# Optimization experiments

Hardware: AMD Instinct MI355X
Metric: run time of the kernel (lower is better)

The kernel has to match this reference:

```python
import jax, jax.numpy as jnp
import numpy as np

D = 1024  # in_features
H = 16    # head_num

def setup_inputs() -> dict:
    key = jax.random.key(0)
    ks = jax.random.split(key, 11)
    S, B = 2048, 2
    scale = 1.0 / np.sqrt(D)
    inp = {
        'q': jax.random.normal(ks[0], (S, B, D), jnp.float32),
        'k': jax.random.normal(ks[1], (S, B, D), jnp.float32),
        'v': jax.random.normal(ks[2], (S, B, D), jnp.float32),
        'Wq': jax.random.normal(ks[3], (D, D), jnp.float32) * scale,
        'Wk': jax.random.normal(ks[4], (D, D), jnp.float32) * scale,
        'Wv': jax.random.normal(ks[5], (D, D), jnp.float32) * scale,
        'Wo': jax.random.normal(ks[6], (D, D), jnp.float32) * scale,
        'bq': jax.random.normal(ks[7], (D,), jnp.float32) * 0.01,
        'bk': jax.random.normal(ks[8], (D,), jnp.float32) * 0.01,
        'bv': jax.random.normal(ks[9], (D,), jnp.float32) * 0.01,
        'bo': jax.random.normal(ks[10], (D,), jnp.float32) * 0.01,
    }
    return inp

def reference(q, k, v, Wq, Wk, Wv, Wo, bq, bk, bv, bo):
    # q,k,v: (S, B, D) -> (B, S, D)
    q = jnp.transpose(q, (1, 0, 2))
    k = jnp.transpose(k, (1, 0, 2))
    v = jnp.transpose(v, (1, 0, 2))
    # linear + ReLU (torch Linear: x @ W.T + b)
    qh = jax.nn.relu(q @ Wq.T + bq)
    kh = jax.nn.relu(k @ Wk.T + bk)
    vh = jax.nn.relu(v @ Wv.T + bv)
    B, S, _ = qh.shape
    hd = D // H
    # (B, S, H, hd) -> (B, H, S, hd)
    qh = qh.reshape(B, S, H, hd).transpose(0, 2, 1, 3)
    kh = kh.reshape(B, S, H, hd).transpose(0, 2, 1, 3)
    vh = vh.reshape(B, S, H, hd).transpose(0, 2, 1, 3)
    scores = jnp.einsum('bhsd,bhtd->bhst', qh, kh) / np.sqrt(hd).astype(np.float32)
    attn = jax.nn.softmax(scores, axis=-1)
    y = jnp.einsum('bhst,bhtd->bhsd', attn, vh)  # (B, H, S, hd)
    y = y.transpose(0, 2, 1, 3).reshape(B, S, D)
    y = jax.nn.relu(y @ Wo.T + bo)
    return jnp.transpose(y, (1, 0, 2))  # (S, B, D)
```

## Files before the change

### kernel.cpp

```cpp
#include <hip/hip_runtime.h>
#include <stdint.h>

typedef __attribute__((ext_vector_type(8))) short bf8v;
typedef __attribute__((ext_vector_type(4))) float f4v;
typedef __attribute__((ext_vector_type(16))) float f16v;
typedef __attribute__((ext_vector_type(4))) unsigned int u4v;

__device__ __forceinline__ unsigned short f2bf(float f) {
  unsigned int u = __float_as_uint(f);
  u += 0x7fffu + ((u >> 16) & 1u);
  return (unsigned short)(u >> 16);
}

__device__ __forceinline__ void gload16(const void* g, void* l) {
  __builtin_amdgcn_global_load_lds(
      (__attribute__((address_space(1))) void*)reinterpret_cast<uintptr_t>(g),
      (__attribute__((address_space(3))) void*)reinterpret_cast<uintptr_t>(l),
      16, 0, 0);
}

__device__ __forceinline__ unsigned cvtpk(float lo, float hi) {
  unsigned r;
  asm("v_cvt_pk_bf16_f32 %0, %1, %2" : "=v"(r) : "v"(lo), "v"(hi));
  return r;
}

__global__ __launch_bounds__(256) void cvt_all(
    const float* __restrict__ s0, const float* __restrict__ s1,
    const float* __restrict__ s2, const float* __restrict__ s3,
    const float* __restrict__ s4, const float* __restrict__ s5,
    const float* __restrict__ s6, unsigned short* __restrict__ dst) {
  const size_t NA = (size_t)1 << 22, NW = (size_t)1 << 20;
  size_t i = ((size_t)blockIdx.x * 256 + threadIdx.x) * 8;
  const float* src;
  size_t off;
  if (i < 3 * NA) {
    int a = (int)(i >> 22);
    src = (a == 0) ? s0 : (a == 1) ? s1 : s2;
    off = i & (NA - 1);
  } else {
    size_t j = i - 3 * NA;
    int a = (int)(j >> 20);
    src = (a == 0) ? s3 : (a == 1) ? s4 : (a == 2) ? s5 : s6;
    off = j & (NW - 1);
  }
  const f4v* sp = (const f4v*)(src + off);
  f4v x = sp[0], y = sp[1];
  bf8v r;
  r[0] = (short)f2bf(x[0]); r[1] = (short)f2bf(x[1]);
  r[2] = (short)f2bf(x[2]); r[3] = (short)f2bf(x[3]);
  r[4] = (short)f2bf(y[0]); r[5] = (short)f2bf(y[1]);
  r[6] = (short)f2bf(y[2]); r[7] = (short)f2bf(y[3]);
  *(bf8v*)(dst + i) = r;
}

template <int OMODE>
__device__ __forceinline__ void gemm_body(
    unsigned short* Al, unsigned short* Bl,
    const unsigned short* __restrict__ A, const unsigned short* __restrict__ W,
    const float* __restrict__ bias, void* __restrict__ out) {
  const int tid = threadIdx.x;
  const int w = tid >> 6, l = tid & 63;
  const int lr = l >> 4, lc = l & 15;
  const int m0 = blockIdx.x * 128, n0 = blockIdx.y * 128;
  const int wr = w >> 1, wc = w & 1;

  f4v acc[4][4];
#pragma unroll
  for (int i = 0; i < 4; i++)
#pragma unroll
    for (int j = 0; j < 4; j++) acc[i][j] = (f4v)(0.0f);

  const int NK = 32;
#pragma unroll
  for (int i = 0; i < 2; i++) {
    int chunk = w * 2 + i;
    int e = (chunk * 1024 + l * 16) >> 1;
    int r = e >> 5, k = e & 31;
    gload16(A + (size_t)(m0 + r) * 1024 + k, Al + chunk * 512);
    gload16(W + (size_t)(n0 + r) * 1024 + k, Bl + chunk * 512);
  }

  for (int kk = 0; kk < NK; kk++) {
    const int cur = kk & 1;
    __syncthreads();
    if (kk + 1 < NK) {
#pragma unroll
      for (int i = 0; i < 2; i++) {
        int chunk = w * 2 + i;
        int e = (chunk * 1024 + l * 16) >> 1;
        int r = e >> 5, k = (kk + 1) * 32 + (e & 31);
        gload16(A + (size_t)(m0 + r) * 1024 + k, Al + (cur ^ 1) * 4096 + chunk * 512);
        gload16(W + (size_t)(n0 + r) * 1024 + k, Bl + (cur ^ 1) * 4096 + chunk * 512);
      }
    }
    bf8v av[4], bv[4];
#pragma unroll
    for (int i = 0; i < 4; i++) {
      int row = wr * 64 + i * 16 + lc;
      av[i] = *(const bf8v*)(Al + cur * 4096 + row * 32 + lr * 8);
    }
#pragma unroll
    for (int j = 0; j < 4; j++) {
      int row = wc * 64 + j * 16 + lc;
      bv[j] = *(const bf8v*)(Bl + cur * 4096 + row * 32 + lr * 8);
    }
#pragma unroll
    for (int i = 0; i < 4; i++)
#pragma unroll
      for (int j = 0; j < 4; j++)
        acc[i][j] = __builtin_amdgcn_mfma_f32_16x16x32_bf16(av[i], bv[j], acc[i][j], 0, 0, 0);
  }

#pragma unroll
  for (int j = 0; j < 4; j++) {
    int n = n0 + wc * 64 + j * 16 + lc;
    float bj = bias[n];
#pragma unroll
    for (int i = 0; i < 4; i++) {
      int mb = m0 + wr * 64 + i * 16 + lr * 4;
#pragma unroll
      for (int q = 0; q < 4; q++) {
        float val = fmaxf(acc[i][j][q] + bj, 0.0f);
        int m = mb + q;
        if (OMODE == 2) {
          int s = m & 2047, b = m >> 11;
          ((float*)out)[(size_t)(s * 2 + b) * 1024 + n] = val;
        } else {
          int s = m >> 1, b = m & 1;
          int h = n >> 6, d = n & 63;
          if (OMODE == 0)
            ((unsigned short*)out)[((size_t)(b * 16 + h) * 2048 + s) * 64 + d] = f2bf(val);
          else
            ((unsigned short*)out)[((size_t)(b * 16 + h) * 64 + d) * 2048 + s] = f2bf(val);
        }
      }
    }
  }
}

__global__ __launch_bounds__(256) void qkv_gemm(
    const unsigned short* __restrict__ qA, const unsigned short* __restrict__ kA,
    const unsigned short* __restrict__ vA,
    const unsigned short* __restrict__ Wq, const unsigned short* __restrict__ Wk,
    const unsigned short* __restrict__ Wv,
    const float* __restrict__ bq, const float* __restrict__ bk,
    const float* __restrict__ bv,
    unsigned short* __restrict__ Qh, unsigned short* __restrict__ Kh,
    unsigned short* __restrict__ Vt) {
  __shared__ __align__(16) unsigned short Al[2 * 4096];
  __shared__ __align__(16) unsigned short Bl[2 * 4096];
  int z = blockIdx.z;
  if (z == 0)      gemm_body<0>(Al, Bl, qA, Wq, bq, Qh);
  else if (z == 1) gemm_body<0>(Al, Bl, kA, Wk, bk, Kh);
  else             gemm_body<1>(Al, Bl, vA, Wv, bv, Vt);
}

__global__ __launch_bounds__(256) void out_gemm(
    const unsigned short* __restrict__ Y, const unsigned short* __restrict__ Wo,
    const float* __restrict__ bo, float* __restrict__ out) {
  __shared__ __align__(16) unsigned short Al[2 * 4096];
  __shared__ __align__(16) unsigned short Bl[2 * 4096];
  gemm_body<2>(Al, Bl, Y, Wo, bo, out);
}

__global__ __launch_bounds__(256, 2) void attn_kernel(
    const unsigned short* __restrict__ Qh, const unsigned short* __restrict__ Kh,
    const unsigned short* __restrict__ Vt, unsigned short* __restrict__ Y) {
  __shared__ __align__(16) unsigned short Kl[2][4096];
  __shared__ __align__(16) unsigned short Vl[2][4096];
  const int tid = threadIdx.x, w = tid >> 6, l = tid & 63;
  const int lo = l & 31, hi = l >> 5;
  const int bh = blockIdx.y;
  const int q0 = blockIdx.x * 128 + w * 32;
  const size_t qkbase = (size_t)bh * 2048 * 64;
  const size_t vtbase = (size_t)bh * 64 * 2048;
  const float cs = 0.125f * 1.44269504088896341f;

  bf8v qf[4];
#pragma unroll
  for (int c = 0; c < 4; c++)
    qf[c] = *(const bf8v*)(Qh + qkbase + (size_t)(q0 + lo) * 64 + c * 16 + hi * 8);

  f16v oacc[2];
  oacc[0] = (f16v)(0.0f);
  oacc[1] = (f16v)(0.0f);
  float mrun = -1e30f, lrun = 0.0f;

  const int swl = (lo & 7) << 4;
  int akb[4], avb[2][2][2];
#pragma unroll
  for (int c = 0; c < 4; c++) akb[c] = lo * 128 + ((c * 32 + hi * 16) ^ swl);
#pragma unroll
  for (int dt = 0; dt < 2; dt++)
#pragma unroll
    for (int kvh = 0; kvh < 2; kvh++)
#pragma unroll
      for (int kc = 0; kc < 2; kc++)
        avb[dt][kvh][kc] = (dt * 32 + lo) * 128 + ((kvh * 64 + kc * 32 + hi * 16) ^ swl);

  int stE[2], stD[2], stKV[2];
#pragma unroll
  for (int i = 0; i < 2; i++) {
    int o = (w * 2 + i) * 1024 + l * 16;
    int row = o >> 7;
    stE[i] = (o ^ ((row & 7) << 4)) >> 1;
    stD[i] = stE[i] >> 6;
    stKV[i] = stE[i] & 63;
  }
  const char* KlB = (const char*)&Kl[0][0];
  const char* VlB = (const char*)&Vl[0][0];

  auto STAGE = [&](int buf, int t0) {
#pragma unroll
    for (int i = 0; i < 2; i++) {
      gload16(Kh + qkbase + (size_t)t0 * 64 + stE[i], (char*)&Kl[buf][0] + (w * 2 + i) * 1024);
      gload16(Vt + vtbase + (size_t)stD[i] * 2048 + t0 + stKV[i], (char*)&Vl[buf][0] + (w * 2 + i) * 1024);
    }
  };

  auto COMPUTE = [&](int bo) {
#pragma unroll
    for (int kvh = 0; kvh < 2; kvh++) {
      bf8v kf[4];
#pragma unroll
      for (int c = 0; c < 4; c++)
        kf[c] = *(const bf8v*)(KlB + bo + kvh * 4096 + akb[c]);
      f16v sc16 = (f16v)(0.0f);
#pragma unroll
      for (int c = 0; c < 4; c++)
        sc16 = __builtin_amdgcn_mfma_f32_32x32x16_bf16(kf[c], qf[c], sc16, 0, 0, 0);
      bf8v vf[2][2];
#pragma unroll
      for (int dt = 0; dt < 2; dt++)
#pragma unroll
        for (int kc = 0; kc < 2; kc++)
          vf[dt][kc] = *(const bf8v*)(VlB + bo + avb[dt][kvh][kc]);

      float m0a = fmaxf(fmaxf(sc16[0], sc16[1]), sc16[2]);
      float m0b = fmaxf(fmaxf(sc16[3], sc16[4]), sc16[5]);
      float m0c = fmaxf(fmaxf(sc16[6], sc16[7]), sc16[8]);
      float m0d = fmaxf(fmaxf(sc16[9], sc16[10]), sc16[11]);
      float m0e = fmaxf(fmaxf(sc16[12], sc16[13]), sc16[14]);
      float m16 = fmaxf(fmaxf(fmaxf(m0a, m0b), fmaxf(m0c, m0d)), fmaxf(m0e, sc16[15]));
      m16 = fmaxf(m16, __shfl_xor(m16, 32));
      float msc = m16 * cs;
      if (!__all(msc <= mrun + 8.0f)) {
        float mnew = fmaxf(mrun, msc);
        float scl = __builtin_amdgcn_exp2f(mrun - mnew);
        lrun *= scl;
#pragma unroll
        for (int dt = 0; dt < 2; dt++)
#pragma unroll
          for (int r = 0; r < 16; r++) oacc[dt][r] *= scl;
        mrun = mnew;
      }
      float p[16];
      float rs = 0.0f;
#pragma unroll
      for (int r = 0; r < 16; r++) {
        p[r] = __builtin_amdgcn_exp2f(sc16[r] * cs - mrun);
        rs += p[r];
      }
      rs += __shfl_xor(rs, 32);
      lrun += rs;
      bf8v pf[2];
#pragma unroll
      for (int kc = 0; kc < 2; kc++) {
        unsigned a0 = cvtpk(p[kc * 8 + 0], p[kc * 8 + 1]);
        unsigned a1 = cvtpk(p[kc * 8 + 2], p[kc * 8 + 3]);
        unsigned b0 = cvtpk(p[kc * 8 + 4], p[kc * 8 + 5]);
        unsigned b1 = cvtpk(p[kc * 8 + 6], p[kc * 8 + 7]);
        asm("v_permlane32_swap_b32 %0, %1" : "+v"(a0), "+v"(b0));
        asm("v_permlane32_swap_b32 %0, %1" : "+v"(a1), "+v"(b1));
        u4v pw;
        pw[0] = a0; pw[1] = a1; pw[2] = b0; pw[3] = b1;
        pf[kc] = __builtin_bit_cast(bf8v, pw);
      }
#pragma unroll
      for (int dt = 0; dt < 2; dt++)
#pragma unroll
        for (int kc = 0; kc < 2; kc++)
          oacc[dt] = __builtin_amdgcn_mfma_f32_32x32x16_bf16(vf[dt][kc], pf[kc], oacc[dt], 0, 0, 0);
    }
  };

  STAGE(0, 0);
  __syncthreads();
#pragma unroll 1
  for (int t0 = 0; t0 < 2048; t0 += 128) {
    STAGE(1, t0 + 64);
    COMPUTE(0);
    __syncthreads();
    if (t0 + 128 < 2048) STAGE(0, t0 + 128);
    COMPUTE(8192);
    __syncthreads();
  }

  const int b = bh >> 4, h = bh & 15;
  {
    float inv = 1.0f / lrun;
    int q = q0 + lo;
    size_t base = ((size_t)(b * 2048 + q) << 10) + h * 64;
#pragma unroll
    for (int dt = 0; dt < 2; dt++)
#pragma unroll
      for (int r = 0; r < 16; r++) {
        int d = dt * 32 + (r & 3) + 8 * (r >> 2) + 4 * hi;
        Y[base + d] = f2bf(oacc[dt][r] * inv);
      }
  }
}

extern "C" void kernel_launch(void* const* d_in, const int* in_sizes, int n_in,
                              void* d_out, int out_size, void* d_ws, size_t ws_size,
                              hipStream_t stream) {
  const float* q  = (const float*)d_in[0];
  const float* k  = (const float*)d_in[1];
  const float* v  = (const float*)d_in[2];
  const float* Wq = (const float*)d_in[3];
  const float* Wk = (const float*)d_in[4];
  const float* Wv = (const float*)d_in[5];
  const float* Wo = (const float*)d_in[6];
  const float* bq = (const float*)d_in[7];
  const float* bk = (const float*)d_in[8];
  const float* bv = (const float*)d_in[9];
  const float* bo = (const float*)d_in[10];

  const size_t NA = (size_t)4096 * 1024;
  const size_t NW = (size_t)1024 * 1024;
  unsigned short* qA  = (unsigned short*)d_ws;
  unsigned short* kA  = qA  + NA;
  unsigned short* vA  = kA  + NA;
  unsigned short* WqB = vA  + NA;
  unsigned short* WkB = WqB + NW;
  unsigned short* WvB = WkB + NW;
  unsigned short* WoB = WvB + NW;
  unsigned short* Qh  = WoB + NW;
  unsigned short* Kh  = Qh  + NA;
  unsigned short* Vt  = Kh  + NA;
  unsigned short* Y   = Vt  + NA;

  cvt_all<<<dim3(8192), 256, 0, stream>>>(q, k, v, Wq, Wk, Wv, Wo, qA);

  qkv_gemm<<<dim3(32, 8, 3), 256, 0, stream>>>(qA, kA, vA, WqB, WkB, WvB,
                                               bq, bk, bv, Qh, Kh, Vt);
  attn_kernel<<<dim3(16, 32), 256, 0, stream>>>(Qh, Kh, Vt, Y);
  out_gemm<<<dim3(32, 8), 256, 0, stream>>>(Y, WoB, bo, (float*)d_out);
}
```

Baseline: 128.5 us.

## Split attention over key range with combine kernel; narrow out_gemm tile

Attention is split into two halves along the key dimension (grid z=2), doubling the block count from 512 to 1024. Each half writes unnormalized partial outputs plus running max/sum, and a new combine kernel merges them into Y. The output GEMM now uses a 64-wide N tile to double its grid, and attention launch bounds request 4 blocks per SM. The aim is better CU occupancy on a 256-CU part, at the cost of an extra kernel launch, extra partial-result traffic, and bf16 rounding of the unnormalized partials.

Measured after the change: 132.3 us. 2.9% more time.

```diff
diff --git a/kernel.cpp b/kernel.cpp
--- a/kernel.cpp
+++ b/kernel.cpp
@@ -10,6 +10,10 @@
   unsigned int u = __float_as_uint(f);
   u += 0x7fffu + ((u >> 16) & 1u);
   return (unsigned short)(u >> 16);
+}
+
+__device__ __forceinline__ float bf2f(unsigned short s) {
+  return __uint_as_float((unsigned)s << 16);
 }
 
 __device__ __forceinline__ void gload16(const void* g, void* l) {
@@ -54,7 +58,7 @@
   *(bf8v*)(dst + i) = r;
 }
 
-template <int OMODE>
+template <int OMODE, int TN>
 __device__ __forceinline__ void gemm_body(
     unsigned short* Al, unsigned short* Bl,
     const unsigned short* __restrict__ A, const unsigned short* __restrict__ W,
@@ -62,22 +66,31 @@
   const int tid = threadIdx.x;
   const int w = tid >> 6, l = tid & 63;
   const int lr = l >> 4, lc = l & 15;
-  const int m0 = blockIdx.x * 128, n0 = blockIdx.y * 128;
+  const int m0 = blockIdx.x * 128, n0 = blockIdx.y * TN;
   const int wr = w >> 1, wc = w & 1;
-
-  f4v acc[4][4];
+  const int JW = TN / 32;
+  const int BCPW = TN / 64;
+  const int BBUF = TN * 32;
+
+  f4v acc[4][JW];
 #pragma unroll
   for (int i = 0; i < 4; i++)
 #pragma unroll
-    for (int j = 0; j < 4; j++) acc[i][j] = (f4v)(0.0f);
+    for (int j = 0; j < JW; j++) acc[i][j] = (f4v)(0.0f);
 
   const int NK = 32;
 #pragma unroll
   for (int i = 0; i < 2; i++) {
     int chunk = w * 2 + i;
-    int e = (chunk * 1024 + l * 16) >> 1;
+    int e = chunk * 512 + l * 8;
     int r = e >> 5, k = e & 31;
     gload16(A + (size_t)(m0 + r) * 1024 + k, Al + chunk * 512);
+  }
+#pragma unroll
+  for (int i = 0; i < BCPW; i++) {
+    int chunk = w * BCPW + i;
+    int e = chunk * 512 + l * 8;
+    int r = e >> 5, k = e & 31;
     gload16(W + (size_t)(n0 + r) * 1024 + k, Bl + chunk * 512);
   }
 
@@ -88,33 +101,39 @@
 #pragma unroll
       for (int i = 0; i < 2; i++) {
         int chunk = w * 2 + i;
-        int e = (chunk * 1024 + l * 16) >> 1;
+        int e = chunk * 512 + l * 8;
         int r = e >> 5, k = (kk + 1) * 32 + (e & 31);
         gload16(A + (size_t)(m0 + r) * 1024 + k, Al + (cur ^ 1) * 4096 + chunk * 512);
-        gload16(W + (size_t)(n0 + r) * 1024 + k, Bl + (cur ^ 1) * 4096 + chunk * 512);
-      }
-    }
-    bf8v av[4], bv[4];
+      }
+#pragma unroll
+      for (int i = 0; i < BCPW; i++) {
+        int chunk = w * BCPW + i;
+        int e = chunk * 512 + l * 8;
+        int r = e >> 5, k = (kk + 1) * 32 + (e & 31);
+        gload16(W + (size_t)(n0 + r) * 1024 + k, Bl + (cur ^ 1) * BBUF + chunk * 512);
+      }
+    }
+    bf8v av[4], bv[JW];
 #pragma unroll
     for (int i = 0; i < 4; i++) {
       int row = wr * 64 + i * 16 + lc;
       av[i] = *(const bf8v*)(Al + cur * 4096 + row * 32 + lr * 8);
     }
 #pragma unroll
-    for (int j = 0; j < 4; j++) {
-      int row = wc * 64 + j * 16 + lc;
-      bv[j] = *(const bf8v*)(Bl + cur * 4096 + row * 32 + lr * 8);
+    for (int j = 0; j < JW; j++) {
+      int row = wc * (TN / 2) + j * 16 + lc;
+      bv[j] = *(const bf8v*)(Bl + cur * BBUF + row * 32 + lr * 8);
     }
 #pragma unroll
     for (int i = 0; i < 4; i++)
 #pragma unroll
-      for (int j = 0; j < 4; j++)
+      for (int j = 0; j < JW; j++)
         acc[i][j] = __builtin_amdgcn_mfma_f32_16x16x32_bf16(av[i], bv[j], acc[i][j], 0, 0, 0);
   }
 
 #pragma unroll
-  for (int j = 0; j < 4; j++) {
-    int n = n0 + wc * 64 + j * 16 + lc;
+  for (int j = 0; j < JW; j++) {
+    int n = n0 + wc * (TN / 2) + j * 16 + lc;
     float bj = bias[n];
 #pragma unroll
     for (int i = 0; i < 4; i++) {
@@ -151,27 +170,30 @@
   __shared__ __align__(16) unsigned short Al[2 * 4096];
   __shared__ __align__(16) unsigned short Bl[2 * 4096];
   int z = blockIdx.z;
-  if (z == 0)      gemm_body<0>(Al, Bl, qA, Wq, bq, Qh);
-  else if (z == 1) gemm_body<0>(Al, Bl, kA, Wk, bk, Kh);
-  else             gemm_body<1>(Al, Bl, vA, Wv, bv, Vt);
+  if (z == 0)      gemm_body<0, 128>(Al, Bl, qA, Wq, bq, Qh);
+  else if (z == 1) gemm_body<0, 128>(Al, Bl, kA, Wk, bk, Kh);
+  else             gemm_body<1, 128>(Al, Bl, vA, Wv, bv, Vt);
 }
 
 __global__ __launch_bounds__(256) void out_gemm(
     const unsigned short* __restrict__ Y, const unsigned short* __restrict__ Wo,
     const float* __restrict__ bo, float* __restrict__ out) {
   __shared__ __align__(16) unsigned short Al[2 * 4096];
-  __shared__ __align__(16) unsigned short Bl[2 * 4096];
-  gemm_body<2>(Al, Bl, Y, Wo, bo, out);
-}
-
-__global__ __launch_bounds__(256, 2) void attn_kernel(
+  __shared__ __align__(16) unsigned short Bl[2 * 2048];
+  gemm_body<2, 64>(Al, Bl, Y, Wo, bo, out);
+}
+
+__global__ __launch_bounds__(256, 4) void attn_kernel(
     const unsigned short* __restrict__ Qh, const unsigned short* __restrict__ Kh,
-    const unsigned short* __restrict__ Vt, unsigned short* __restrict__ Y) {
+    const unsigned short* __restrict__ Vt,
+    unsigned short* __restrict__ PO, float2* __restrict__ ML) {
   __shared__ __align__(16) unsigned short Kl[2][4096];
   __shared__ __align__(16) unsigned short Vl[2][4096];
   const int tid = threadIdx.x, w = tid >> 6, l = tid & 63;
   const int lo = l & 31, hi = l >> 5;
   const int bh = blockIdx.y;
+  const int z = blockIdx.z;
+  const int tbeg = z << 10, tend = tbeg + 1024;
   const int q0 = blockIdx.x * 128 + w * 32;
   const size_t qkbase = (size_t)bh * 2048 * 64;
   const size_t vtbase = (size_t)bh * 64 * 2048;
@@ -285,30 +307,59 @@
     }
   };
 
-  STAGE(0, 0);
+  STAGE(0, tbeg);
   __syncthreads();
 #pragma unroll 1
-  for (int t0 = 0; t0 < 2048; t0 += 128) {
+  for (int t0 = tbeg; t0 < tend; t0 += 128) {
     STAGE(1, t0 + 64);
     COMPUTE(0);
     __syncthreads();
-    if (t0 + 128 < 2048) STAGE(0, t0 + 128);
+    if (t0 + 128 < tend) STAGE(0, t0 + 128);
     COMPUTE(8192);
     __syncthreads();
   }
 
-  const int b = bh >> 4, h = bh & 15;
   {
-    float inv = 1.0f / lrun;
     int q = q0 + lo;
-    size_t base = ((size_t)(b * 2048 + q) << 10) + h * 64;
+    size_t prow = (size_t)(z * 32 + bh) * 2048 + q;
+    if (hi == 0) ML[prow] = float2{mrun, lrun};
+    unsigned short* pp = PO + prow * 64;
 #pragma unroll
     for (int dt = 0; dt < 2; dt++)
 #pragma unroll
       for (int r = 0; r < 16; r++) {
         int d = dt * 32 + (r & 3) + 8 * (r >> 2) + 4 * hi;
-        Y[base + d] = f2bf(oacc[dt][r] * inv);
-      }
+        pp[d] = f2bf(oacc[dt][r]);
+      }
+  }
+}
+
+__global__ __launch_bounds__(256) void combine_kernel(
+    const unsigned short* __restrict__ PO, const float2* __restrict__ ML,
+    unsigned short* __restrict__ Y) {
+  int idx = blockIdx.x * 256 + threadIdx.x;
+  int row = idx >> 1, hr = idx & 1;
+  int bh = row >> 11, q = row & 2047;
+  float2 ml0 = ML[row], ml1 = ML[65536 + row];
+  float M = fmaxf(ml0.x, ml1.x);
+  float a0 = __builtin_amdgcn_exp2f(ml0.x - M);
+  float a1 = __builtin_amdgcn_exp2f(ml1.x - M);
+  float L = ml0.y * a0 + ml1.y * a1;
+  float s0 = a0 / L, s1 = a1 / L;
+  const unsigned short* p0 = PO + (size_t)row * 64 + hr * 32;
+  const unsigned short* p1 = PO + ((size_t)65536 + row) * 64 + hr * 32;
+  int b = bh >> 4, h = bh & 15;
+  unsigned short* yp = Y + (((size_t)(b * 2048 + q)) << 10) + h * 64 + hr * 32;
+#pragma unroll
+  for (int g = 0; g < 4; g++) {
+    bf8v v0 = *(const bf8v*)(p0 + g * 8);
+    bf8v v1 = *(const bf8v*)(p1 + g * 8);
+    bf8v r;
+#pragma unroll
+    for (int j = 0; j < 8; j++)
+      r[j] = (short)f2bf(bf2f((unsigned short)v0[j]) * s0 +
+                         bf2f((unsigned short)v1[j]) * s1);
+    *(bf8v*)(yp + g * 8) = r;
   }
 }
 
@@ -341,10 +392,14 @@
   unsigned short* Vt  = Kh  + NA;
   unsigned short* Y   = Vt  + NA;
 
+  unsigned short* PO = qA;
+  float2*         ML = (float2*)vA;
+
   cvt_all<<<dim3(8192), 256, 0, stream>>>(q, k, v, Wq, Wk, Wv, Wo, qA);
 
   qkv_gemm<<<dim3(32, 8, 3), 256, 0, stream>>>(qA, kA, vA, WqB, WkB, WvB,
                                                bq, bk, bv, Qh, Kh, Vt);
-  attn_kernel<<<dim3(16, 32), 256, 0, stream>>>(Qh, Kh, Vt, Y);
-  out_gemm<<<dim3(32, 8), 256, 0, stream>>>(Y, WoB, bo, (float*)d_out);
-}
+  attn_kernel<<<dim3(16, 32, 2), 256, 0, stream>>>(Qh, Kh, Vt, PO, ML);
+  combine_kernel<<<dim3(512), 256, 0, stream>>>(PO, ML, Y);
+  out_gemm<<<dim3(32, 16), 256, 0, stream>>>(Y, WoB, bo, (float*)d_out);
+}
```
